# Kernel optimization log

Hardware: AMD Instinct MI355X
Metric: run time of the kernel (lower is better)

The kernel has to match this reference:

```python
import jax, jax.numpy as jnp
import numpy as np

B = 64          # number of trees (batch)
N = 131072      # total nodes in batch
H_ENC = 512
H_DEC = 512


def setup_inputs() -> dict:
    key = jax.random.key(0)
    k1, k2, k3, k4, k5 = jax.random.split(key, 5)
    hidden_states = jax.random.normal(k1, (B, H_DEC), dtype=jnp.float32)
    encoder_output = jax.random.normal(k2, (N, H_ENC), dtype=jnp.float32)
    # sorted segment ids encode ragged tree membership (same info as tree_sizes)
    segment_ids = jnp.sort(jax.random.randint(k3, (N,), 0, B)).astype(jnp.int32)
    # linear: nn.Linear(h_dec + h_enc, h_enc, bias=False) -> weight [h_enc, h_dec+h_enc]
    W = jax.random.normal(k4, (H_ENC, H_DEC + H_ENC), dtype=jnp.float32) / np.float32(np.sqrt(H_DEC + H_ENC))
    # v: torch.rand(h_enc, 1)
    v = jax.random.uniform(k5, (H_ENC, 1), dtype=jnp.float32)
    return {"hidden_states": hidden_states, "encoder_output": encoder_output,
            "segment_ids": segment_ids, "W": W, "v": v}


def reference(hidden_states, encoder_output, segment_ids, W, v):
    # repeat each tree's decoder state over its nodes: [N, h_dec]
    repeated = hidden_states[segment_ids]
    # concat score: tanh(Linear([h_dec ; h_enc])) @ v
    cat = jnp.concatenate([repeated, encoder_output], axis=1)      # [N, h_dec+h_enc]
    energy = jnp.tanh(cat @ W.T)                                   # [N, h_enc]
    scores = energy @ v                                            # [N, 1]
    s = scores[:, 0]
    # segment-wise (per-tree) softmax over ragged node groups
    seg_max = jax.ops.segment_max(s, segment_ids, num_segments=B)
    e = jnp.exp(s - seg_max[segment_ids])
    denom = jax.ops.segment_sum(e, segment_ids, num_segments=B)
    att = e / denom[segment_ids]
    return att[:, None]                                            # [N, 1]
```

## Files before the change

kernel.cpp:

```cpp
#include <hip/hip_runtime.h>
#include <math.h>

#define NROWS 131072
#define NSEG  64
#define HH    512

typedef unsigned short u16;
typedef unsigned int   u32;
typedef __attribute__((ext_vector_type(8))) short short8;
typedef __attribute__((ext_vector_type(8))) u16   us8;
typedef __attribute__((ext_vector_type(4))) float f32x4;
typedef __attribute__((ext_vector_type(4))) u32   u32x4;

__device__ __forceinline__ u32 f2u(float f){ union {float f; u32 u;} c; c.f=f; return c.u; }
__device__ __forceinline__ float u2f(u32 u){ union {u32 u; float f;} c; c.u=u; return c.f; }
__device__ __forceinline__ u16 bf16_rne(float f){
  u32 u = f2u(f);
  u32 r = u + 0x7FFFu + ((u >> 16) & 1u);
  return (u16)(r >> 16);
}
__device__ __forceinline__ float fast_tanh(float x){
  float e = __expf(2.0f * x);
  return 1.0f - __fdividef(2.0f, e + 1.0f);
}
__device__ __forceinline__ void gload_lds16(const void* g, void* l) {
  __builtin_amdgcn_global_load_lds((const __attribute__((address_space(1))) void*)g,
                                   (__attribute__((address_space(3))) void*)l, 16, 0, 0);
}

__global__ __launch_bounds__(256)
void hproj_kernel(const float* __restrict__ hidden, const float* __restrict__ W,
                  float* __restrict__ hproj)
{
  const int b    = blockIdx.x;
  const int tid  = threadIdx.x;
  const int wave = tid >> 6;
  const int lane = tid & 63;
  const float* hrow = hidden + (size_t)b * HH + lane * 8;
  const float4 h0 = *(const float4*)(hrow);
  const float4 h1 = *(const float4*)(hrow + 4);
  for (int j = wave; j < HH; j += 4) {
    const float* wrow = W + (size_t)j * 1024 + lane * 8;
    const float4 w0 = *(const float4*)(wrow);
    const float4 w1 = *(const float4*)(wrow + 4);
    float acc = h0.x*w0.x + h0.y*w0.y + h0.z*w0.z + h0.w*w0.w
              + h1.x*w1.x + h1.y*w1.y + h1.z*w1.z + h1.w*w1.w;
    #pragma unroll
    for (int o = 32; o; o >>= 1) acc += __shfl_xor(acc, o);
    if (lane == 0) hproj[(size_t)b * HH + j] = acc;
  }
}

__global__ __launch_bounds__(256)
void w2split_kernel(const float* __restrict__ W, u16* __restrict__ hi, u16* __restrict__ lo)
{
  const int idx = blockIdx.x * 256 + threadIdx.x;
  const int j = idx >> 9, k = idx & 511;
  const float x = W[(size_t)j * 1024 + 512 + k];
  const u32 u = f2u(x);
  hi[idx] = (u16)(u >> 16);
  lo[idx] = bf16_rne(x - u2f(u & 0xFFFF0000u));
}

__global__ __launch_bounds__(256, 3)
void gemm_fused_kernel(const float* __restrict__ enc,
                       const u16* __restrict__ w2hi, const u16* __restrict__ w2lo,
                       const float* __restrict__ hproj, const float* __restrict__ vvec,
                       const int* __restrict__ seg, float* __restrict__ scores)
{
  __shared__ float sAf[128 * 32];
  __shared__ u16   sBh[128 * 32];
  __shared__ u16   sBl[128 * 32];

  const int tid  = threadIdx.x;
  const int bx   = blockIdx.x;
  const int row0 = (bx >> 2) * 128;
  const int col0 = (bx & 3) * 128;

  const int wave = tid >> 6;
  const int lane = tid & 63;
  const int wr   = (wave >> 1) * 64;
  const int wc   = (wave & 1) * 64;
  const int l15  = lane & 15;
  const int quad = lane >> 4;

  const int arow = tid >> 3;
  const int acol = ((tid & 7) ^ (arow & 6)) * 4;
  const float* gA = enc + (size_t)(row0 + arow) * HH + acol;
  const int awb = (tid >> 6) * 256;

  const int brow = tid >> 2;
  const int bcol = ((tid & 3) ^ ((brow >> 1) & 3)) * 8;
  const u16* gBh = w2hi + (size_t)(col0 + brow) * HH + bcol;
  const u16* gBl = w2lo + (size_t)(col0 + brow) * HH + bcol;
  const int bwb = (tid >> 6) * 512;

  f32x4 acc[4][4];
  #pragma unroll
  for (int i = 0; i < 4; i++)
    #pragma unroll
    for (int j = 0; j < 4; j++)
      acc[i][j] = (f32x4){0.f, 0.f, 0.f, 0.f};

  for (int ks = 0; ks < HH; ks += 32) {
    #pragma unroll
    for (int i = 0; i < 4; i++)
      gload_lds16(gA + (size_t)i * 32 * HH + ks, &sAf[i * 1024 + awb]);
    gload_lds16(gBh + ks,                      &sBh[bwb]);
    gload_lds16(gBh + (size_t)64 * HH + ks,    &sBh[2048 + bwb]);
    gload_lds16(gBl + ks,                      &sBl[bwb]);
    gload_lds16(gBl + (size_t)64 * HH + ks,    &sBl[2048 + bwb]);
    __syncthreads();

    short8 bhf[4], blf[4];
    #pragma unroll
    for (int j = 0; j < 4; j++) {
      const int r  = wc + j * 16 + l15;
      const int off = r * 32 + 8 * (quad ^ ((r >> 1) & 3));
      bhf[j] = *(const short8*)&sBh[off];
      blf[j] = *(const short8*)&sBl[off];
    }

    #pragma unroll
    for (int i = 0; i < 4; i++) {
      const int r  = wr + i * 16 + l15;
      const int ab = r * 32 + 8 * (quad ^ ((r >> 1) & 3));
      const f32x4 x0 = *(const f32x4*)&sAf[ab];
      const f32x4 x1 = *(const f32x4*)&sAf[ab + 4];
      union { u32x4 w; short8 s; } ah, al;
      #pragma unroll
      for (int p = 0; p < 4; p++) {
        const float xa = (p < 2) ? x0[2 * p] : x1[2 * p - 4];
        const float xb = (p < 2) ? x0[2 * p + 1] : x1[2 * p - 3];
        const u32 ua = f2u(xa), ub = f2u(xb);
        ah.w[p] = (ua >> 16) | (ub & 0xFFFF0000u);
        const float ra = xa - u2f(ua & 0xFFFF0000u);
        const float rb = xb - u2f(ub & 0xFFFF0000u);
        al.w[p] = (f2u(ra) >> 16) | (f2u(rb) & 0xFFFF0000u);
      }
      #pragma unroll
      for (int j = 0; j < 4; j++) {
        acc[i][j] = __builtin_amdgcn_mfma_f32_16x16x32_bf16(ah.s, bhf[j], acc[i][j], 0, 0, 0);
        acc[i][j] = __builtin_amdgcn_mfma_f32_16x16x32_bf16(al.s, bhf[j], acc[i][j], 0, 0, 0);
        acc[i][j] = __builtin_amdgcn_mfma_f32_16x16x32_bf16(ah.s, blf[j], acc[i][j], 0, 0, 0);
      }
    }
    __syncthreads();
  }

  int   jn[4];
  float vv[4];
  #pragma unroll
  for (int j = 0; j < 4; j++) { jn[j] = col0 + wc + j * 16 + l15; vv[j] = vvec[jn[j]]; }

  #pragma unroll
  for (int i = 0; i < 4; i++) {
    #pragma unroll
    for (int r = 0; r < 4; r++) {
      const int gn = row0 + wr + i * 16 + quad * 4 + r;
      const float* hp = hproj + (size_t)seg[gn] * HH;
      float p = 0.f;
      #pragma unroll
      for (int j = 0; j < 4; j++) {
        const float c = acc[i][j][r] + hp[jn[j]];
        p += fast_tanh(c) * vv[j];
      }
      p += __shfl_xor(p, 1);
      p += __shfl_xor(p, 2);
      p += __shfl_xor(p, 4);
      p += __shfl_xor(p, 8);
      if (l15 == 0) atomicAdd(&scores[gn], p);
    }
  }
}

__global__ __launch_bounds__(256)
void seg_softmax_kernel(const float* __restrict__ scores, const int* __restrict__ seg,
                        float* __restrict__ out)
{
  const int b    = blockIdx.x;
  const int tid  = threadIdx.x;
  const int wv   = tid >> 6;
  const int lane = tid & 63;
  __shared__ float red[4];

  int lo = 0, hi = NROWS;
  while (lo < hi) { int mid = (lo + hi) >> 1; if (seg[mid] < b) lo = mid + 1; else hi = mid; }
  const int start = lo;
  lo = 0; hi = NROWS;
  while (lo < hi) { int mid = (lo + hi) >> 1; if (seg[mid] < b + 1) lo = mid + 1; else hi = mid; }
  const int end = lo;

  float lm = -3.4e38f;
  for (int i = start + tid; i < end; i += 256) lm = fmaxf(lm, scores[i]);
  #pragma unroll
  for (int o = 32; o; o >>= 1) lm = fmaxf(lm, __shfl_xor(lm, o));
  if (lane == 0) red[wv] = lm;
  __syncthreads();
  const float gm = fmaxf(fmaxf(red[0], red[1]), fmaxf(red[2], red[3]));
  __syncthreads();

  float ls = 0.f;
  for (int i = start + tid; i < end; i += 256) ls += expf(scores[i] - gm);
  #pragma unroll
  for (int o = 32; o; o >>= 1) ls += __shfl_xor(ls, o);
  if (lane == 0) red[wv] = ls;
  __syncthreads();
  const float denom = red[0] + red[1] + red[2] + red[3];
  const float inv = 1.0f / denom;

  for (int i = start + tid; i < end; i += 256) out[i] = expf(scores[i] - gm) * inv;
}

extern "C" void kernel_launch(void* const* d_in, const int* in_sizes, int n_in,
                              void* d_out, int out_size, void* d_ws, size_t ws_size,
                              hipStream_t stream)
{
  const float* hidden = (const float*)d_in[0];
  const float* enc    = (const float*)d_in[1];
  const int*   seg    = (const int*)d_in[2];
  const float* W      = (const float*)d_in[3];
  const float* vvec   = (const float*)d_in[4];
  float* out = (float*)d_out;

  float* scores = (float*)d_ws;
  float* hproj  = scores + NROWS;
  u16*   w2hi   = (u16*)(hproj + NSEG * HH);
  u16*   w2lo   = w2hi + (size_t)HH * HH;

  hipMemsetAsync(scores, 0, NROWS * sizeof(float), stream);
  hproj_kernel<<<NSEG, 256, 0, stream>>>(hidden, W, hproj);
  w2split_kernel<<<(HH * HH) / 256, 256, 0, stream>>>(W, w2hi, w2lo);
  gemm_fused_kernel<<<(NROWS / 128) * 4, 256, 0, stream>>>(enc, w2hi, w2lo,
                                                           hproj, vvec, seg, scores);
  seg_softmax_kernel<<<NSEG, 256, 0, stream>>>(scores, seg, out);
}
```

Measured before the change: 646.1 us.

## Widen GEMM tile to 128x256 and split hproj across more blocks

```diff
diff --git a/kernel.cpp b/kernel.cpp
--- a/kernel.cpp
+++ b/kernel.cpp
@@ -32,14 +32,15 @@
 void hproj_kernel(const float* __restrict__ hidden, const float* __restrict__ W,
                   float* __restrict__ hproj)
 {
-  const int b    = blockIdx.x;
+  const int b    = blockIdx.x >> 2;
+  const int q    = blockIdx.x & 3;
   const int tid  = threadIdx.x;
   const int wave = tid >> 6;
   const int lane = tid & 63;
   const float* hrow = hidden + (size_t)b * HH + lane * 8;
   const float4 h0 = *(const float4*)(hrow);
   const float4 h1 = *(const float4*)(hrow + 4);
-  for (int j = wave; j < HH; j += 4) {
+  for (int j = q * 128 + wave; j < q * 128 + 128; j += 4) {
     const float* wrow = W + (size_t)j * 1024 + lane * 8;
     const float4 w0 = *(const float4*)(wrow);
     const float4 w1 = *(const float4*)(wrow + 4);
@@ -62,25 +63,25 @@
   lo[idx] = bf16_rne(x - u2f(u & 0xFFFF0000u));
 }
 
-__global__ __launch_bounds__(256, 3)
+__global__ __launch_bounds__(256, 2)
 void gemm_fused_kernel(const float* __restrict__ enc,
                        const u16* __restrict__ w2hi, const u16* __restrict__ w2lo,
                        const float* __restrict__ hproj, const float* __restrict__ vvec,
                        const int* __restrict__ seg, float* __restrict__ scores)
 {
   __shared__ float sAf[128 * 32];
-  __shared__ u16   sBh[128 * 32];
-  __shared__ u16   sBl[128 * 32];
+  __shared__ u16   sBh[256 * 32];
+  __shared__ u16   sBl[256 * 32];
 
   const int tid  = threadIdx.x;
   const int bx   = blockIdx.x;
-  const int row0 = (bx >> 2) * 128;
-  const int col0 = (bx & 3) * 128;
+  const int row0 = (bx >> 1) * 128;
+  const int col0 = (bx & 1) * 256;
 
   const int wave = tid >> 6;
   const int lane = tid & 63;
-  const int wr   = (wave >> 1) * 64;
-  const int wc   = (wave & 1) * 64;
+  const int wrow = (wave >> 1) * 64;
+  const int wcol = (wave & 1) * 128;
   const int l15  = lane & 15;
   const int quad = lane >> 4;
 
@@ -95,73 +96,77 @@
   const u16* gBl = w2lo + (size_t)(col0 + brow) * HH + bcol;
   const int bwb = (tid >> 6) * 512;
 
-  f32x4 acc[4][4];
+  f32x4 acc[4][8];
   #pragma unroll
   for (int i = 0; i < 4; i++)
     #pragma unroll
-    for (int j = 0; j < 4; j++)
+    for (int j = 0; j < 8; j++)
       acc[i][j] = (f32x4){0.f, 0.f, 0.f, 0.f};
 
   for (int ks = 0; ks < HH; ks += 32) {
     #pragma unroll
     for (int i = 0; i < 4; i++)
       gload_lds16(gA + (size_t)i * 32 * HH + ks, &sAf[i * 1024 + awb]);
-    gload_lds16(gBh + ks,                      &sBh[bwb]);
-    gload_lds16(gBh + (size_t)64 * HH + ks,    &sBh[2048 + bwb]);
-    gload_lds16(gBl + ks,                      &sBl[bwb]);
-    gload_lds16(gBl + (size_t)64 * HH + ks,    &sBl[2048 + bwb]);
+    #pragma unroll
+    for (int i = 0; i < 4; i++)
+      gload_lds16(gBh + (size_t)i * 64 * HH + ks, &sBh[i * 2048 + bwb]);
+    #pragma unroll
+    for (int i = 0; i < 4; i++)
+      gload_lds16(gBl + (size_t)i * 64 * HH + ks, &sBl[i * 2048 + bwb]);
     __syncthreads();
 
-    short8 bhf[4], blf[4];
-    #pragma unroll
-    for (int j = 0; j < 4; j++) {
-      const int r  = wc + j * 16 + l15;
-      const int off = r * 32 + 8 * (quad ^ ((r >> 1) & 3));
-      bhf[j] = *(const short8*)&sBh[off];
-      blf[j] = *(const short8*)&sBl[off];
-    }
-
+    short8 ah[4], al[4];
     #pragma unroll
     for (int i = 0; i < 4; i++) {
-      const int r  = wr + i * 16 + l15;
-      const int ab = r * 32 + 8 * (quad ^ ((r >> 1) & 3));
+      const int r  = wrow + i * 16 + l15;
+      const int ab = r * 32 + (((2 * quad) ^ (r & 6))) * 4;
       const f32x4 x0 = *(const f32x4*)&sAf[ab];
       const f32x4 x1 = *(const f32x4*)&sAf[ab + 4];
-      union { u32x4 w; short8 s; } ah, al;
+      union { u32x4 w; short8 s; } H, L;
       #pragma unroll
       for (int p = 0; p < 4; p++) {
         const float xa = (p < 2) ? x0[2 * p] : x1[2 * p - 4];
         const float xb = (p < 2) ? x0[2 * p + 1] : x1[2 * p - 3];
         const u32 ua = f2u(xa), ub = f2u(xb);
-        ah.w[p] = (ua >> 16) | (ub & 0xFFFF0000u);
+        H.w[p] = __builtin_amdgcn_perm(ub, ua, 0x07060302u);
         const float ra = xa - u2f(ua & 0xFFFF0000u);
         const float rb = xb - u2f(ub & 0xFFFF0000u);
-        al.w[p] = (f2u(ra) >> 16) | (f2u(rb) & 0xFFFF0000u);
+        L.w[p] = __builtin_amdgcn_perm(f2u(rb), f2u(ra), 0x07060302u);
       }
+      ah[i] = H.s;
+      al[i] = L.s;
+    }
+
+    #pragma unroll
+    for (int j = 0; j < 8; j++) {
+      const int rr  = wcol + j * 16 + l15;
+      const int off = rr * 32 + (quad ^ ((rr >> 1) & 3)) * 8;
+      const short8 bh = *(const short8*)&sBh[off];
+      const short8 bl = *(const short8*)&sBl[off];
       #pragma unroll
-      for (int j = 0; j < 4; j++) {
-        acc[i][j] = __builtin_amdgcn_mfma_f32_16x16x32_bf16(ah.s, bhf[j], acc[i][j], 0, 0, 0);
-        acc[i][j] = __builtin_amdgcn_mfma_f32_16x16x32_bf16(al.s, bhf[j], acc[i][j], 0, 0, 0);
-        acc[i][j] = __builtin_amdgcn_mfma_f32_16x16x32_bf16(ah.s, blf[j], acc[i][j], 0, 0, 0);
+      for (int i = 0; i < 4; i++) {
+        acc[i][j] = __builtin_amdgcn_mfma_f32_16x16x32_bf16(ah[i], bh, acc[i][j], 0, 0, 0);
+        acc[i][j] = __builtin_amdgcn_mfma_f32_16x16x32_bf16(al[i], bh, acc[i][j], 0, 0, 0);
+        acc[i][j] = __builtin_amdgcn_mfma_f32_16x16x32_bf16(ah[i], bl, acc[i][j], 0, 0, 0);
       }
     }
     __syncthreads();
   }
 
-  int   jn[4];
-  float vv[4];
-  #pragma unroll
-  for (int j = 0; j < 4; j++) { jn[j] = col0 + wc + j * 16 + l15; vv[j] = vvec[jn[j]]; }
+  int   jn[8];
+  float vv[8];
+  #pragma unroll
+  for (int j = 0; j < 8; j++) { jn[j] = col0 + wcol + j * 16 + l15; vv[j] = vvec[jn[j]]; }
 
   #pragma unroll
   for (int i = 0; i < 4; i++) {
     #pragma unroll
     for (int r = 0; r < 4; r++) {
-      const int gn = row0 + wr + i * 16 + quad * 4 + r;
+      const int gn = row0 + wrow + i * 16 + quad * 4 + r;
       const float* hp = hproj + (size_t)seg[gn] * HH;
       float p = 0.f;
       #pragma unroll
-      for (int j = 0; j < 4; j++) {
+      for (int j = 0; j < 8; j++) {
         const float c = acc[i][j][r] + hp[jn[j]];
         p += fast_tanh(c) * vv[j];
       }
@@ -229,9 +234,9 @@
   u16*   w2lo   = w2hi + (size_t)HH * HH;
 
   hipMemsetAsync(scores, 0, NROWS * sizeof(float), stream);
-  hproj_kernel<<<NSEG, 256, 0, stream>>>(hidden, W, hproj);
+  hproj_kernel<<<NSEG * 4, 256, 0, stream>>>(hidden, W, hproj);
   w2split_kernel<<<(HH * HH) / 256, 256, 0, stream>>>(W, w2hi, w2lo);
-  gemm_fused_kernel<<<(NROWS / 128) * 4, 256, 0, stream>>>(enc, w2hi, w2lo,
+  gemm_fused_kernel<<<(NROWS / 128) * 2, 256, 0, stream>>>(enc, w2hi, w2lo,
                                                            hproj, vvec, seg, scores);
   seg_softmax_kernel<<<NSEG, 256, 0, stream>>>(scores, seg, out);
 }
```

Result: faster. 543.1 us (-15.9%).
